# Kernel optimization log

Hardware: AMD Instinct MI355X
Metric: run time of the kernel (lower is better)

## Reference

```python
import jax, jax.numpy as jnp
import numpy as np

STATE_DIM = 4096
HIDDEN_DIM = 4096
GRU_STEP = 8
N_NODES = 4


def setup_inputs() -> dict:
    key = jax.random.key(0)
    ks = jax.random.split(key, 8)
    s = STATE_DIM
    scale = 0.02  # keep gate pre-activations in a sane range
    return {
        "A_out": jax.random.uniform(ks[0], (N_NODES, N_NODES), dtype=jnp.float32),
        "A_in": jax.random.uniform(ks[1], (N_NODES, N_NODES), dtype=jnp.float32),
        "annotation": jax.random.normal(ks[2], (N_NODES, s), dtype=jnp.float32),
        "W_ih": jax.random.normal(ks[3], (3 * s, 2 * s), dtype=jnp.float32) * scale,
        "W_hh": jax.random.normal(ks[4], (3 * s, s), dtype=jnp.float32) * scale,
        "fc1_w": jax.random.normal(ks[5], (HIDDEN_DIM, N_NODES * s), dtype=jnp.float32) * scale,
        "fc1_b": jnp.zeros((HIDDEN_DIM,), dtype=jnp.float32),
        "fc2_w": jax.random.normal(ks[6], (2, HIDDEN_DIM), dtype=jnp.float32) * scale,
        "fc2_b": jnp.zeros((2,), dtype=jnp.float32),
    }


def _gru_cell(x, h, W_ih, W_hh):
    # PyTorch GRUCell (bias=False), gate order r, z, n
    gi = x @ W_ih.T  # [N, 3*s]
    gh = h @ W_hh.T  # [N, 3*s]
    i_r, i_z, i_n = jnp.split(gi, 3, axis=1)
    h_r, h_z, h_n = jnp.split(gh, 3, axis=1)
    r = jax.nn.sigmoid(i_r + h_r)
    z = jax.nn.sigmoid(i_z + h_z)
    n = jnp.tanh(i_n + r * h_n)
    return (1.0 - z) * n + z * h


def reference(A_out, A_in, annotation, W_ih, W_hh, fc1_w, fc1_b, fc2_w, fc2_b):
    def step(h, _):
        a = jnp.concatenate((A_out @ h, A_in @ h), axis=1)  # [N, 2*s]
        return _gru_cell(a, h, W_ih, W_hh), None

    h, _ = jax.lax.scan(step, annotation, None, length=GRU_STEP)
    enc = h.reshape(1, -1)  # [1, N*s]
    x = enc @ fc1_w.T + fc1_b
    x = x @ fc2_w.T + fc2_b
    return jax.nn.log_softmax(x, axis=1)
```

## Files before the change

kernel.cpp:

```cpp
#include <hip/hip_runtime.h>
#include <hip/hip_bf16.h>
#include <math.h>


#define S 4096

__device__ __forceinline__ float wave_reduce_add(float v) {
#pragma unroll
    for (int off = 32; off > 0; off >>= 1) v += __shfl_down(v, off, 64);
    return v;
}

__global__ void init_h_k(const float* __restrict__ ann, float4* __restrict__ h) {
    int k = blockIdx.x * 256 + threadIdx.x;
    float4 o;
    o.x = ann[k];
    o.y = ann[S + k];
    o.z = ann[2 * S + k];
    o.w = ann[3 * S + k];
    h[k] = o;
}

__global__ void compute_a_k(const float* __restrict__ Aout, const float* __restrict__ Ain,
                            const float4* __restrict__ h, float4* __restrict__ a) {
    int k = blockIdx.x * 256 + threadIdx.x;
    const float* M = (k < S) ? Aout : Ain;
    int kk = k & (S - 1);
    float4 hv = h[kk];
    float4 o;
    o.x = M[0]  * hv.x + M[1]  * hv.y + M[2]  * hv.z + M[3]  * hv.w;
    o.y = M[4]  * hv.x + M[5]  * hv.y + M[6]  * hv.z + M[7]  * hv.w;
    o.z = M[8]  * hv.x + M[9]  * hv.y + M[10] * hv.z + M[11] * hv.w;
    o.w = M[12] * hv.x + M[13] * hv.y + M[14] * hv.z + M[15] * hv.w;
    a[k] = o;
}

__global__ __launch_bounds__(256) void gru_col_k(
    const float* __restrict__ Wih, const float* __restrict__ Whh,
    const float4* __restrict__ a, const float4* __restrict__ hcur,
    float4* __restrict__ hnext) {
    const int c = blockIdx.x;
    const int t = threadIdx.x;

    float accI[3][4];
    float accH[3][4];
#pragma unroll
    for (int g = 0; g < 3; g++)
#pragma unroll
        for (int n = 0; n < 4; n++) { accI[g][n] = 0.f; accH[g][n] = 0.f; }

    const float4* Wi[3];
    Wi[0] = (const float4*)(Wih + (size_t)(0 * S + c) * (2 * S));
    Wi[1] = (const float4*)(Wih + (size_t)(1 * S + c) * (2 * S));
    Wi[2] = (const float4*)(Wih + (size_t)(2 * S + c) * (2 * S));

#pragma unroll 2
    for (int i = 0; i < 8; i++) {
        int j = t + 256 * i;
        int ka = 4 * j;
        float4 a0 = a[ka + 0];
        float4 a1 = a[ka + 1];
        float4 a2 = a[ka + 2];
        float4 a3 = a[ka + 3];
#pragma unroll
        for (int g = 0; g < 3; g++) {
            float4 w = Wi[g][j];
            accI[g][0] += w.x * a0.x + w.y * a1.x + w.z * a2.x + w.w * a3.x;
            accI[g][1] += w.x * a0.y + w.y * a1.y + w.z * a2.y + w.w * a3.y;
            accI[g][2] += w.x * a0.z + w.y * a1.z + w.z * a2.z + w.w * a3.z;
            accI[g][3] += w.x * a0.w + w.y * a1.w + w.z * a2.w + w.w * a3.w;
        }
    }

    const float4* Wh[3];
    Wh[0] = (const float4*)(Whh + (size_t)(0 * S + c) * S);
    Wh[1] = (const float4*)(Whh + (size_t)(1 * S + c) * S);
    Wh[2] = (const float4*)(Whh + (size_t)(2 * S + c) * S);

#pragma unroll 2
    for (int i = 0; i < 4; i++) {
        int j = t + 256 * i;
        int ka = 4 * j;
        float4 h0 = hcur[ka + 0];
        float4 h1 = hcur[ka + 1];
        float4 h2 = hcur[ka + 2];
        float4 h3 = hcur[ka + 3];
#pragma unroll
        for (int g = 0; g < 3; g++) {
            float4 w = Wh[g][j];
            accH[g][0] += w.x * h0.x + w.y * h1.x + w.z * h2.x + w.w * h3.x;
            accH[g][1] += w.x * h0.y + w.y * h1.y + w.z * h2.y + w.w * h3.y;
            accH[g][2] += w.x * h0.z + w.y * h1.z + w.z * h2.z + w.w * h3.z;
            accH[g][3] += w.x * h0.w + w.y * h1.w + w.z * h2.w + w.w * h3.w;
        }
    }

    __shared__ float red[4][24];
    int lane = t & 63, wid = t >> 6;
#pragma unroll
    for (int g = 0; g < 3; g++) {
#pragma unroll
        for (int n = 0; n < 4; n++) {
            float vI = wave_reduce_add(accI[g][n]);
            float vH = wave_reduce_add(accH[g][n]);
            if (lane == 0) {
                red[wid][g * 4 + n] = vI;
                red[wid][12 + g * 4 + n] = vH;
            }
        }
    }
    __syncthreads();

    if (t < 4) {
        int n = t;
        float I[3], H[3];
#pragma unroll
        for (int g = 0; g < 3; g++) {
            I[g] = red[0][g * 4 + n] + red[1][g * 4 + n] + red[2][g * 4 + n] + red[3][g * 4 + n];
            H[g] = red[0][12 + g * 4 + n] + red[1][12 + g * 4 + n] + red[2][12 + g * 4 + n] + red[3][12 + g * 4 + n];
        }
        float r = 1.f / (1.f + expf(-(I[0] + H[0])));
        float z = 1.f / (1.f + expf(-(I[1] + H[1])));
        float nn = tanhf(I[2] + r * H[2]);
        float hv = ((const float*)hcur)[c * 4 + n];
        ((float*)hnext)[c * 4 + n] = (1.f - z) * nn + z * hv;
    }
}

__global__ void enc_k(const float4* __restrict__ h, float* __restrict__ enc) {
    int idx = blockIdx.x * 256 + threadIdx.x;
    int n = idx >> 12;
    int k = idx & (S - 1);
    enc[idx] = ((const float*)h)[k * 4 + n];
}

__global__ __launch_bounds__(256) void fc1_k(const float* __restrict__ W, const float* __restrict__ b,
                                             const float* __restrict__ enc, float* __restrict__ x1) {
    int j = blockIdx.x, t = threadIdx.x;
    const float4* row = (const float4*)(W + (size_t)j * (4 * S));
    const float4* e4 = (const float4*)enc;
    float acc = 0.f;
#pragma unroll 4
    for (int i = 0; i < 16; i++) {
        int m = t + 256 * i;
        float4 w = row[m];
        float4 e = e4[m];
        acc += w.x * e.x + w.y * e.y + w.z * e.z + w.w * e.w;
    }
    acc = wave_reduce_add(acc);
    __shared__ float red[4];
    if ((t & 63) == 0) red[t >> 6] = acc;
    __syncthreads();
    if (t == 0) x1[j] = red[0] + red[1] + red[2] + red[3] + b[j];
}

__global__ __launch_bounds__(256) void fc2_k(const float* __restrict__ W, const float* __restrict__ b,
                                             const float* __restrict__ x1, float* __restrict__ out) {
    int t = threadIdx.x;
    const float4* x4 = (const float4*)x1;
    const float4* w0 = (const float4*)W;
    const float4* w1 = (const float4*)(W + S);
    float a0 = 0.f, a1 = 0.f;
#pragma unroll
    for (int i = 0; i < 4; i++) {
        int m = t + 256 * i;
        float4 x = x4[m];
        float4 u = w0[m];
        float4 v = w1[m];
        a0 += u.x * x.x + u.y * x.y + u.z * x.z + u.w * x.w;
        a1 += v.x * x.x + v.y * x.y + v.z * x.z + v.w * x.w;
    }
    a0 = wave_reduce_add(a0);
    a1 = wave_reduce_add(a1);
    __shared__ float red0[4], red1[4];
    int lane = t & 63, wid = t >> 6;
    if (lane == 0) { red0[wid] = a0; red1[wid] = a1; }
    __syncthreads();
    if (t == 0) {
        float l0 = red0[0] + red0[1] + red0[2] + red0[3] + b[0];
        float l1 = red1[0] + red1[1] + red1[2] + red1[3] + b[1];
        float m = fmaxf(l0, l1);
        float ls = m + logf(expf(l0 - m) + expf(l1 - m));
        out[0] = l0 - ls;
        out[1] = l1 - ls;
    }
}

extern "C" void kernel_launch(void* const* d_in, const int* in_sizes, int n_in,
                              void* d_out, int out_size, void* d_ws, size_t ws_size,
                              hipStream_t stream) {
    const float* A_out = (const float*)d_in[0];
    const float* A_in  = (const float*)d_in[1];
    const float* ann   = (const float*)d_in[2];
    const float* W_ih  = (const float*)d_in[3];
    const float* W_hh  = (const float*)d_in[4];
    const float* fc1_w = (const float*)d_in[5];
    const float* fc1_b = (const float*)d_in[6];
    const float* fc2_w = (const float*)d_in[7];
    const float* fc2_b = (const float*)d_in[8];
    float* out = (float*)d_out;

    float* ws_f = (float*)d_ws;
    float4* hA  = (float4*)ws_f;
    float4* hB  = hA + S;
    float4* a_t = hB + S;
    float* enc  = (float*)(a_t + 2 * S);
    float* x1   = enc + 4 * S;

    init_h_k<<<S / 256, 256, 0, stream>>>(ann, hA);

    for (int step = 0; step < 8; step++) {
        float4* cur = (step & 1) ? hB : hA;
        float4* nxt = (step & 1) ? hA : hB;
        compute_a_k<<<2 * S / 256, 256, 0, stream>>>(A_out, A_in, cur, a_t);
        gru_col_k<<<S, 256, 0, stream>>>(W_ih, W_hh, a_t, cur, nxt);
    }
    enc_k<<<4 * S / 256, 256, 0, stream>>>(hA, enc);
    fc1_k<<<S, 256, 0, stream>>>(fc1_w, fc1_b, enc, x1);
    fc2_k<<<1, 256, 0, stream>>>(fc2_w, fc2_b, x1, out);
}
```

Before: 1.678 ms.

## Convert GRU weights to bf16 in first step and reuse for later steps

On the first GRU step a fused kernel computes the fp32 matvec and also writes bf16-packed copies of W_ih and W_hh to workspace. Steps 2-8 then read the half-size bf16 weights, which roughly halves the dominant weight bandwidth per step (the weights total about 600MB in fp32, far beyond cache). The cost is extra writes in step 0, bf16 rounding error in the gate pre-activations, and a much larger workspace requirement.

```diff
diff --git a/kernel.cpp b/kernel.cpp
--- a/kernel.cpp
+++ b/kernel.cpp
@@ -10,6 +10,16 @@
     for (int off = 32; off > 0; off >>= 1) v += __shfl_down(v, off, 64);
     return v;
 }
+
+__device__ __forceinline__ unsigned pack_bf16_rn(float lo, float hi) {
+    unsigned a = __float_as_uint(lo);
+    unsigned b = __float_as_uint(hi);
+    a = (a + 0x7FFFu + ((a >> 16) & 1u)) >> 16;
+    b = (b + 0x7FFFu + ((b >> 16) & 1u)) & 0xFFFF0000u;
+    return a | b;
+}
+__device__ __forceinline__ float bf_lo(unsigned u) { return __uint_as_float(u << 16); }
+__device__ __forceinline__ float bf_hi(unsigned u) { return __uint_as_float(u & 0xFFFF0000u); }
 
 __global__ void init_h_k(const float* __restrict__ ann, float4* __restrict__ h) {
     int k = blockIdx.x * 256 + threadIdx.x;
@@ -35,66 +45,9 @@
     a[k] = o;
 }
 
-__global__ __launch_bounds__(256) void gru_col_k(
-    const float* __restrict__ Wih, const float* __restrict__ Whh,
-    const float4* __restrict__ a, const float4* __restrict__ hcur,
-    float4* __restrict__ hnext) {
-    const int c = blockIdx.x;
-    const int t = threadIdx.x;
-
-    float accI[3][4];
-    float accH[3][4];
-#pragma unroll
-    for (int g = 0; g < 3; g++)
-#pragma unroll
-        for (int n = 0; n < 4; n++) { accI[g][n] = 0.f; accH[g][n] = 0.f; }
-
-    const float4* Wi[3];
-    Wi[0] = (const float4*)(Wih + (size_t)(0 * S + c) * (2 * S));
-    Wi[1] = (const float4*)(Wih + (size_t)(1 * S + c) * (2 * S));
-    Wi[2] = (const float4*)(Wih + (size_t)(2 * S + c) * (2 * S));
-
-#pragma unroll 2
-    for (int i = 0; i < 8; i++) {
-        int j = t + 256 * i;
-        int ka = 4 * j;
-        float4 a0 = a[ka + 0];
-        float4 a1 = a[ka + 1];
-        float4 a2 = a[ka + 2];
-        float4 a3 = a[ka + 3];
-#pragma unroll
-        for (int g = 0; g < 3; g++) {
-            float4 w = Wi[g][j];
-            accI[g][0] += w.x * a0.x + w.y * a1.x + w.z * a2.x + w.w * a3.x;
-            accI[g][1] += w.x * a0.y + w.y * a1.y + w.z * a2.y + w.w * a3.y;
-            accI[g][2] += w.x * a0.z + w.y * a1.z + w.z * a2.z + w.w * a3.z;
-            accI[g][3] += w.x * a0.w + w.y * a1.w + w.z * a2.w + w.w * a3.w;
-        }
-    }
-
-    const float4* Wh[3];
-    Wh[0] = (const float4*)(Whh + (size_t)(0 * S + c) * S);
-    Wh[1] = (const float4*)(Whh + (size_t)(1 * S + c) * S);
-    Wh[2] = (const float4*)(Whh + (size_t)(2 * S + c) * S);
-
-#pragma unroll 2
-    for (int i = 0; i < 4; i++) {
-        int j = t + 256 * i;
-        int ka = 4 * j;
-        float4 h0 = hcur[ka + 0];
-        float4 h1 = hcur[ka + 1];
-        float4 h2 = hcur[ka + 2];
-        float4 h3 = hcur[ka + 3];
-#pragma unroll
-        for (int g = 0; g < 3; g++) {
-            float4 w = Wh[g][j];
-            accH[g][0] += w.x * h0.x + w.y * h1.x + w.z * h2.x + w.w * h3.x;
-            accH[g][1] += w.x * h0.y + w.y * h1.y + w.z * h2.y + w.w * h3.y;
-            accH[g][2] += w.x * h0.z + w.y * h1.z + w.z * h2.z + w.w * h3.z;
-            accH[g][3] += w.x * h0.w + w.y * h1.w + w.z * h2.w + w.w * h3.w;
-        }
-    }
-
+__device__ __forceinline__ void gru_epilogue(
+    float accI[3][4], float accH[3][4], int c, int t,
+    const float4* hcur, float4* hnext) {
     __shared__ float red[4][24];
     int lane = t & 63, wid = t >> 6;
 #pragma unroll
@@ -110,7 +63,6 @@
         }
     }
     __syncthreads();
-
     if (t < 4) {
         int n = t;
         float I[3], H[3];
@@ -125,6 +77,155 @@
         float hv = ((const float*)hcur)[c * 4 + n];
         ((float*)hnext)[c * 4 + n] = (1.f - z) * nn + z * hv;
     }
+}
+
+__global__ __launch_bounds__(256) void gru_conv_k(
+    const float* __restrict__ Wih, const float* __restrict__ Whh,
+    uint4* __restrict__ Wib, uint4* __restrict__ Whhb,
+    const float4* __restrict__ a, const float4* __restrict__ hcur,
+    float4* __restrict__ hnext) {
+    const int c = blockIdx.x;
+    const int t = threadIdx.x;
+
+    float accI[3][4], accH[3][4];
+#pragma unroll
+    for (int g = 0; g < 3; g++)
+#pragma unroll
+        for (int n = 0; n < 4; n++) { accI[g][n] = 0.f; accH[g][n] = 0.f; }
+
+    const float4* Wi[3];
+    uint4* Wo[3];
+#pragma unroll
+    for (int g = 0; g < 3; g++) {
+        Wi[g] = (const float4*)(Wih + (size_t)(g * S + c) * (2 * S));
+        Wo[g] = Wib + (size_t)(g * S + c) * 1024;
+    }
+#pragma unroll 1
+    for (int i = 0; i < 4; i++) {
+        int jc = t + 256 * i;
+        float4 av[8];
+#pragma unroll
+        for (int m = 0; m < 8; m++) av[m] = a[8 * jc + m];
+#pragma unroll
+        for (int g = 0; g < 3; g++) {
+            float4 w0 = Wi[g][2 * jc];
+            float4 w1 = Wi[g][2 * jc + 1];
+            uint4 p;
+            p.x = pack_bf16_rn(w0.x, w0.y);
+            p.y = pack_bf16_rn(w0.z, w0.w);
+            p.z = pack_bf16_rn(w1.x, w1.y);
+            p.w = pack_bf16_rn(w1.z, w1.w);
+            Wo[g][jc] = p;
+            accI[g][0] += w0.x * av[0].x + w0.y * av[1].x + w0.z * av[2].x + w0.w * av[3].x
+                        + w1.x * av[4].x + w1.y * av[5].x + w1.z * av[6].x + w1.w * av[7].x;
+            accI[g][1] += w0.x * av[0].y + w0.y * av[1].y + w0.z * av[2].y + w0.w * av[3].y
+                        + w1.x * av[4].y + w1.y * av[5].y + w1.z * av[6].y + w1.w * av[7].y;
+            accI[g][2] += w0.x * av[0].z + w0.y * av[1].z + w0.z * av[2].z + w0.w * av[3].z
+                        + w1.x * av[4].z + w1.y * av[5].z + w1.z * av[6].z + w1.w * av[7].z;
+            accI[g][3] += w0.x * av[0].w + w0.y * av[1].w + w0.z * av[2].w + w0.w * av[3].w
+                        + w1.x * av[4].w + w1.y * av[5].w + w1.z * av[6].w + w1.w * av[7].w;
+        }
+    }
+
+    const float4* Wh[3];
+    uint4* Who[3];
+#pragma unroll
+    for (int g = 0; g < 3; g++) {
+        Wh[g] = (const float4*)(Whh + (size_t)(g * S + c) * S);
+        Who[g] = Whhb + (size_t)(g * S + c) * 512;
+    }
+#pragma unroll 1
+    for (int i = 0; i < 2; i++) {
+        int jc = t + 256 * i;
+        float4 hv[8];
+#pragma unroll
+        for (int m = 0; m < 8; m++) hv[m] = hcur[8 * jc + m];
+#pragma unroll
+        for (int g = 0; g < 3; g++) {
+            float4 w0 = Wh[g][2 * jc];
+            float4 w1 = Wh[g][2 * jc + 1];
+            uint4 p;
+            p.x = pack_bf16_rn(w0.x, w0.y);
+            p.y = pack_bf16_rn(w0.z, w0.w);
+            p.z = pack_bf16_rn(w1.x, w1.y);
+            p.w = pack_bf16_rn(w1.z, w1.w);
+            Who[g][jc] = p;
+            accH[g][0] += w0.x * hv[0].x + w0.y * hv[1].x + w0.z * hv[2].x + w0.w * hv[3].x
+                        + w1.x * hv[4].x + w1.y * hv[5].x + w1.z * hv[6].x + w1.w * hv[7].x;
+            accH[g][1] += w0.x * hv[0].y + w0.y * hv[1].y + w0.z * hv[2].y + w0.w * hv[3].y
+                        + w1.x * hv[4].y + w1.y * hv[5].y + w1.z * hv[6].y + w1.w * hv[7].y;
+            accH[g][2] += w0.x * hv[0].z + w0.y * hv[1].z + w0.z * hv[2].z + w0.w * hv[3].z
+                        + w1.x * hv[4].z + w1.y * hv[5].z + w1.z * hv[6].z + w1.w * hv[7].z;
+            accH[g][3] += w0.x * hv[0].w + w0.y * hv[1].w + w0.z * hv[2].w + w0.w * hv[3].w
+                        + w1.x * hv[4].w + w1.y * hv[5].w + w1.z * hv[6].w + w1.w * hv[7].w;
+        }
+    }
+
+    gru_epilogue(accI, accH, c, t, hcur, hnext);
+}
+
+#define DOT8(ACC, W, AV)                                                                   \
+    ACC[0] += bf_lo(W.x) * AV[0].x + bf_hi(W.x) * AV[1].x + bf_lo(W.y) * AV[2].x +         \
+              bf_hi(W.y) * AV[3].x + bf_lo(W.z) * AV[4].x + bf_hi(W.z) * AV[5].x +         \
+              bf_lo(W.w) * AV[6].x + bf_hi(W.w) * AV[7].x;                                 \
+    ACC[1] += bf_lo(W.x) * AV[0].y + bf_hi(W.x) * AV[1].y + bf_lo(W.y) * AV[2].y +         \
+              bf_hi(W.y) * AV[3].y + bf_lo(W.z) * AV[4].y + bf_hi(W.z) * AV[5].y +         \
+              bf_lo(W.w) * AV[6].y + bf_hi(W.w) * AV[7].y;                                 \
+    ACC[2] += bf_lo(W.x) * AV[0].z + bf_hi(W.x) * AV[1].z + bf_lo(W.y) * AV[2].z +         \
+              bf_hi(W.y) * AV[3].z + bf_lo(W.z) * AV[4].z + bf_hi(W.z) * AV[5].z +         \
+              bf_lo(W.w) * AV[6].z + bf_hi(W.w) * AV[7].z;                                 \
+    ACC[3] += bf_lo(W.x) * AV[0].w + bf_hi(W.x) * AV[1].w + bf_lo(W.y) * AV[2].w +         \
+              bf_hi(W.y) * AV[3].w + bf_lo(W.z) * AV[4].w + bf_hi(W.z) * AV[5].w +         \
+              bf_lo(W.w) * AV[6].w + bf_hi(W.w) * AV[7].w;
+
+__global__ __launch_bounds__(256, 4) void gru_bf16_k(
+    const uint4* __restrict__ Wib, const uint4* __restrict__ Whhb,
+    const float4* __restrict__ a, const float4* __restrict__ hcur,
+    float4* __restrict__ hnext) {
+    const int c = blockIdx.x;
+    const int t = threadIdx.x;
+
+    float accI[3][4], accH[3][4];
+#pragma unroll
+    for (int g = 0; g < 3; g++)
+#pragma unroll
+        for (int n = 0; n < 4; n++) { accI[g][n] = 0.f; accH[g][n] = 0.f; }
+
+    const uint4* Wi[3];
+#pragma unroll
+    for (int g = 0; g < 3; g++) Wi[g] = Wib + (size_t)(g * S + c) * 1024;
+
+#pragma unroll 1
+    for (int i = 0; i < 4; i++) {
+        int jc = t + 256 * i;
+        float4 av[8];
+#pragma unroll
+        for (int m = 0; m < 8; m++) av[m] = a[8 * jc + m];
+#pragma unroll
+        for (int g = 0; g < 3; g++) {
+            uint4 w = Wi[g][jc];
+            DOT8(accI[g], w, av)
+        }
+    }
+
+    const uint4* Wh[3];
+#pragma unroll
+    for (int g = 0; g < 3; g++) Wh[g] = Whhb + (size_t)(g * S + c) * 512;
+
+#pragma unroll 1
+    for (int i = 0; i < 2; i++) {
+        int jc = t + 256 * i;
+        float4 hv[8];
+#pragma unroll
+        for (int m = 0; m < 8; m++) hv[m] = hcur[8 * jc + m];
+#pragma unroll
+        for (int g = 0; g < 3; g++) {
+            uint4 w = Wh[g][jc];
+            DOT8(accH[g], w, hv)
+        }
+    }
+
+    gru_epilogue(accI, accH, c, t, hcur, hnext);
 }
 
 __global__ void enc_k(const float4* __restrict__ h, float* __restrict__ enc) {
@@ -200,8 +301,11 @@
     const float* fc2_b = (const float*)d_in[8];
     float* out = (float*)d_out;
 
-    float* ws_f = (float*)d_ws;
-    float4* hA  = (float4*)ws_f;
+    char* ws = (char*)d_ws;
+    uint4* Wib  = (uint4*)ws;
+    uint4* Whhb = (uint4*)(ws + (size_t)12288 * 1024 * 16);
+    char* ws2 = ws + (size_t)12288 * 1024 * 16 + (size_t)12288 * 512 * 16;
+    float4* hA  = (float4*)ws2;
     float4* hB  = hA + S;
     float4* a_t = hB + S;
     float* enc  = (float*)(a_t + 2 * S);
@@ -213,7 +317,11 @@
         float4* cur = (step & 1) ? hB : hA;
         float4* nxt = (step & 1) ? hA : hB;
         compute_a_k<<<2 * S / 256, 256, 0, stream>>>(A_out, A_in, cur, a_t);
-        gru_col_k<<<S, 256, 0, stream>>>(W_ih, W_hh, a_t, cur, nxt);
+        if (step == 0) {
+            gru_conv_k<<<S, 256, 0, stream>>>(W_ih, W_hh, Wib, Whhb, a_t, cur, nxt);
+        } else {
+            gru_bf16_k<<<S, 256, 0, stream>>>(Wib, Whhb, a_t, cur, nxt);
+        }
     }
     enc_k<<<4 * S / 256, 256, 0, stream>>>(hA, enc);
     fc1_k<<<S, 256, 0, stream>>>(fc1_w, fc1_b, enc, x1);
```

After: 2.096 ms. 1.25x slower.
